# Performance work log

Measured on AMD Instinct MI355X. Metric: run time of the kernel, lower is better.

## Reference

```python
import jax, jax.numpy as jnp
import numpy as np

N_HEAD = 16
HEAD_DIM = 128
HIDDEN = 2048
ROPE_BASE = 10000.0
RMS_EPS = 1e-5


def _rms_norm(t, w, eps=RMS_EPS):
    # RMSNorm over last dim with learned scale
    var = jnp.mean(jnp.square(t), axis=-1, keepdims=True)
    return t * jax.lax.rsqrt(var + eps) * w


def _rope_cos_sin(T, dim, base=ROPE_BASE, dtype=jnp.float32):
    inv_freq = 1.0 / (base ** (jnp.arange(0, dim, 2, dtype=jnp.float32) / dim))
    pos = jnp.arange(T, dtype=jnp.float32)
    freqs = pos[:, None] * inv_freq[None, :]  # [T, dim/2]
    return jnp.cos(freqs).astype(dtype), jnp.sin(freqs).astype(dtype)


def _apply_rotary(t, cos, sin):
    # t: [B, T, H, D]; rotate-half (GPT-NeoX style)
    d2 = t.shape[-1] // 2
    t1, t2 = t[..., :d2], t[..., d2:]
    c = cos[None, :, None, :]
    s = sin[None, :, None, :]
    return jnp.concatenate([t1 * c - t2 * s, t1 * s + t2 * c], axis=-1)


def setup_inputs() -> dict:
    key = jax.random.key(0)
    ks = jax.random.split(key, 7)
    B, T = 2, 2048
    w_std = 1.0 / np.sqrt(HIDDEN)
    proj_std = 0.5 / np.sqrt(HIDDEN) / np.sqrt(24)  # hidden_init_std_factor / sqrt(H) / sqrt(L)
    return {
        "x": jax.random.normal(ks[0], (B, T, HIDDEN), jnp.float32),
        "Wq": jax.random.normal(ks[1], (HIDDEN, N_HEAD * HEAD_DIM), jnp.float32) * w_std,
        "Wk": jax.random.normal(ks[2], (HIDDEN, N_HEAD * HEAD_DIM), jnp.float32) * w_std,
        "Wv": jax.random.normal(ks[3], (HIDDEN, N_HEAD * HEAD_DIM), jnp.float32) * w_std,
        "Wg": jax.random.normal(ks[4], (HIDDEN, N_HEAD * HEAD_DIM), jnp.float32) * w_std,
        "Wo": jax.random.normal(ks[5], (N_HEAD * HEAD_DIM, HIDDEN), jnp.float32) * proj_std,
        "q_rms_w": jnp.ones((HEAD_DIM,), jnp.float32),
        "k_rms_w": jnp.ones((HEAD_DIM,), jnp.float32),
        "o_norm_w": jnp.ones((HEAD_DIM,), jnp.float32),
    }


def reference(x, Wq, Wk, Wv, Wg, Wo, q_rms_w, k_rms_w, o_norm_w):
    B, T, _ = x.shape
    H, D = N_HEAD, HEAD_DIM

    q = (x @ Wq).reshape(B, T, H, D)
    k = (x @ Wk).reshape(B, T, H, D)
    v = (x @ Wv).reshape(B, T, H, D)

    # RoPE (no past, offset = 0)
    cos, sin = _rope_cos_sin(T, D, dtype=x.dtype)
    q = _apply_rotary(q, cos, sin)
    k = _apply_rotary(k, cos, sin)

    # QK RMSNorm (per-head-dim affine)
    q = _rms_norm(q, q_rms_w)
    k = _rms_norm(k, k_rms_w)

    # causal SDPA
    scale = 1.0 / np.sqrt(D)
    scores = jnp.einsum("bqhd,bkhd->bhqk", q, k) * scale
    causal = jnp.tril(jnp.ones((T, T), dtype=bool))
    scores = jnp.where(causal[None, None, :, :], scores, jnp.finfo(scores.dtype).min)
    probs = jax.nn.softmax(scores, axis=-1)
    y = jnp.einsum("bhqk,bkhd->bqhd", probs, v)  # [B, T, H, D]

    # output norm + silu gate
    y = _rms_norm(y, o_norm_w)
    gate = (x @ Wg).reshape(B, T, H, D)
    y = y * jax.nn.silu(gate)

    y = y.reshape(B, T, H * D)
    return y @ Wo
```

## Files before the change

### kernel.cpp

```cpp
#include <hip/hip_runtime.h>
#include <hip/hip_bf16.h>
#include <stdint.h>

typedef __bf16 bf16x8 __attribute__((ext_vector_type(8)));
typedef float f32x4 __attribute__((ext_vector_type(4)));
typedef __hip_bfloat16 bf16;

__device__ __forceinline__ void gload16(const void* g, void* l) {
    __builtin_amdgcn_global_load_lds(
        (const __attribute__((address_space(1))) uint32_t*)g,
        (__attribute__((address_space(3))) uint32_t*)l,
        16, 0, 0);
}

__global__ void k_cvt_bf16(const float* __restrict__ in, bf16* __restrict__ out, int n4) {
    int i = blockIdx.x * blockDim.x + threadIdx.x;
    if (i >= n4) return;
    float4 v = reinterpret_cast<const float4*>(in)[i];
    union { bf16 h[4]; uint2 u; } pk;
    pk.h[0] = __float2bfloat16(v.x);
    pk.h[1] = __float2bfloat16(v.y);
    pk.h[2] = __float2bfloat16(v.z);
    pk.h[3] = __float2bfloat16(v.w);
    reinterpret_cast<uint2*>(out)[i] = pk.u;
}

__global__ void k_rope_tbl(float* __restrict__ tbl) {
    int i = blockIdx.x * blockDim.x + threadIdx.x;
    int t = i >> 6, j = i & 63;
    float inv = powf(10000.0f, -(float)j * (1.0f / 64.0f));
    float f = (float)t * inv;
    tbl[t * 128 + j] = cosf(f);
    tbl[t * 128 + 64 + j] = sinf(f);
}

__global__ void k_wtrans(const float* __restrict__ w0, const float* __restrict__ w1,
                         const float* __restrict__ w2, const float* __restrict__ w3,
                         const float* __restrict__ w4, bf16* __restrict__ out) {
    __shared__ float tile[32][33];
    const float* srcs[5] = {w0, w1, w2, w3, w4};
    const float* src = srcs[blockIdx.z];
    bf16* dst = out + (size_t)blockIdx.z * 2048 * 2048;
    int k0 = blockIdx.x * 32, n0 = blockIdx.y * 32;
    int tx = threadIdx.x, ty = threadIdx.y;
#pragma unroll
    for (int i = 0; i < 4; i++)
        tile[ty + 8 * i][tx] = src[(size_t)(k0 + ty + 8 * i) * 2048 + n0 + tx];
    __syncthreads();
#pragma unroll
    for (int i = 0; i < 4; i++)
        dst[(size_t)(n0 + ty + 8 * i) * 2048 + k0 + tx] = __float2bfloat16(tile[tx][ty + 8 * i]);
}

__global__ __launch_bounds__(256) void k_gemm(
    const bf16* __restrict__ A, const bf16* __restrict__ Bt, float* __restrict__ C,
    int M, int N, int K) {
    __shared__ __align__(16) bf16 As[128 * 64];
    __shared__ __align__(16) bf16 Bs[128 * 64];
    int lane = threadIdx.x & 63, wave = threadIdx.x >> 6;
    int g = lane >> 4, cc = lane & 15;
    int wr = wave >> 1, wc = wave & 1;
    size_t m0 = (size_t)blockIdx.x * 128, n0 = (size_t)blockIdx.y * 128;
    const bf16* Ab = A + m0 * K;
    const bf16* Bb = Bt + (size_t)blockIdx.z * N * K + n0 * K;
    float* Cb = C + (size_t)blockIdx.z * M * N + m0 * N + n0;

    f32x4 acc[4][4];
#pragma unroll
    for (int i = 0; i < 4; i++)
#pragma unroll
        for (int j = 0; j < 4; j++) acc[i][j] = {0.f, 0.f, 0.f, 0.f};

    int scol = (lane & 7) * 8;
    for (int k0 = 0; k0 < K; k0 += 64) {
#pragma unroll
        for (int i = 0; i < 4; i++) {
            int ch = wave * 4 + i;
            int row = ch * 8 + (lane >> 3);
            gload16(&Ab[(size_t)row * K + k0 + scol], &As[ch * 512]);
            gload16(&Bb[(size_t)row * K + k0 + scol], &Bs[ch * 512]);
        }
        __syncthreads();
#pragma unroll
        for (int kk = 0; kk < 2; kk++) {
            bf16x8 af[4], bfr[4];
#pragma unroll
            for (int m = 0; m < 4; m++)
                af[m] = *reinterpret_cast<const bf16x8*>(&As[(wr * 64 + m * 16 + cc) * 64 + kk * 32 + g * 8]);
#pragma unroll
            for (int n = 0; n < 4; n++)
                bfr[n] = *reinterpret_cast<const bf16x8*>(&Bs[(wc * 64 + n * 16 + cc) * 64 + kk * 32 + g * 8]);
#pragma unroll
            for (int m = 0; m < 4; m++)
#pragma unroll
                for (int n = 0; n < 4; n++)
                    acc[m][n] = __builtin_amdgcn_mfma_f32_16x16x32_bf16(af[m], bfr[n], acc[m][n], 0, 0, 0);
        }
        __syncthreads();
    }
#pragma unroll
    for (int m = 0; m < 4; m++)
#pragma unroll
        for (int n = 0; n < 4; n++)
#pragma unroll
            for (int r = 0; r < 4; r++) {
                size_t row = wr * 64 + m * 16 + g * 4 + r;
                Cb[row * N + (wc * 64 + n * 16 + cc)] = acc[m][n][r];
            }
}

__global__ __launch_bounds__(512, 2) void k_gemm256(
    const bf16* __restrict__ A, const bf16* __restrict__ Bt, bf16* __restrict__ C,
    int M, int N, int K) {
    __shared__ __align__(16) bf16 lds[2][8][64 * 64];
    const int tid = threadIdx.x;
    const int lane = tid & 63, wave = tid >> 6;
    const int g = lane >> 4, c = lane & 15, cx = c & 7;
    const int wr = wave >> 2, wc = wave & 3;
    const int id = blockIdx.x;
    const int swz = (id & 7) * 64 + (id >> 3);
    const int xt = swz & 15, yt = (swz >> 4) & 7, zt = swz >> 7;
    const size_t m0 = (size_t)xt * 256, n0 = (size_t)yt * 256;
    const bf16* Ab = A + m0 * K;
    const bf16* Bb = Bt + (size_t)zt * (size_t)N * K + n0 * K;
    bf16* Cb = C + (size_t)zt * (size_t)M * N + m0 * N + n0;
    const int nt = K >> 6;

    const int srow = tid >> 3;
    const int scol = ((tid & 7) ^ (srow & 7)) * 8;

    auto stage = [&](int u, int q) {
        if (u >= nt) return;
        const bf16* src = (q < 4) ? &Ab[(size_t)(q * 64 + srow) * K]
                                  : &Bb[(size_t)((q - 4) * 64 + srow) * K];
        gload16(&src[((size_t)u << 6) + scol], &lds[u & 1][q][wave * 512]);
    };

    f32x4 acc[8][4];
#pragma unroll
    for (int i = 0; i < 8; i++)
#pragma unroll
        for (int j = 0; j < 4; j++) acc[i][j] = {0.f, 0.f, 0.f, 0.f};

#pragma unroll
    for (int q = 0; q < 8; q++) stage(0, q);
    stage(1, 0); stage(1, 2); stage(1, 4); stage(1, 5); stage(1, 6); stage(1, 7);
    asm volatile("s_waitcnt vmcnt(6)" ::: "memory");
    __builtin_amdgcn_s_barrier();

    bf16x8 afr[4][2], bfr[2][2][2];

#define READ_A(mh)                                                                   \
    do {                                                                             \
        const bf16* aq = &lds[t & 1][wr * 2 + (mh)][0];                              \
        _Pragma("unroll") for (int m_ = 0; m_ < 4; m_++)                             \
            _Pragma("unroll") for (int kh = 0; kh < 2; kh++)                         \
                afr[m_][kh] = *reinterpret_cast<const bf16x8*>(                      \
                    aq + (m_ * 16 + c) * 64 + ((kh * 4 + g) ^ cx) * 8);              \
    } while (0)
#define READ_B(nh)                                                                   \
    do {                                                                             \
        const bf16* bq = &lds[t & 1][4 + wc][0];                                     \
        _Pragma("unroll") for (int n_ = 0; n_ < 2; n_++)                             \
            _Pragma("unroll") for (int kh = 0; kh < 2; kh++)                         \
                bfr[nh][n_][kh] = *reinterpret_cast<const bf16x8*>(                  \
                    bq + (((nh)*2 + n_) * 16 + c) * 64 + ((kh * 4 + g) ^ cx) * 8);   \
    } while (0)
#define QUAD(mh, nh)                                                                 \
    do {                                                                             \
        __builtin_amdgcn_s_setprio(1);                                               \
        _Pragma("unroll") for (int kh = 0; kh < 2; kh++)                             \
            _Pragma("unroll") for (int m_ = 0; m_ < 4; m_++)                         \
                _Pragma("unroll") for (int n_ = 0; n_ < 2; n_++)                     \
                    acc[(mh)*4 + m_][(nh)*2 + n_] =                                  \
                        __builtin_amdgcn_mfma_f32_16x16x32_bf16(                     \
                            afr[m_][kh], bfr[nh][n_][kh],                            \
                            acc[(mh)*4 + m_][(nh)*2 + n_], 0, 0, 0);                 \
        __builtin_amdgcn_s_setprio(0);                                               \
    } while (0)

    for (int t = 0; t < nt; ++t) {
        READ_A(0);
        READ_B(0);
        stage(t + 1, 1); stage(t + 1, 3);
        __builtin_amdgcn_s_barrier();
        asm volatile("s_waitcnt lgkmcnt(0)" ::: "memory");
        __builtin_amdgcn_sched_barrier(0);
        QUAD(0, 0);
        __builtin_amdgcn_s_barrier();
        READ_B(1);
        stage(t + 2, 0); stage(t + 2, 2);
        __builtin_amdgcn_s_barrier();
        asm volatile("s_waitcnt lgkmcnt(0)" ::: "memory");
        __builtin_amdgcn_sched_barrier(0);
        QUAD(0, 1);
        __builtin_amdgcn_s_barrier();
        READ_A(1);
        stage(t + 2, 4); stage(t + 2, 5);
        __builtin_amdgcn_s_barrier();
        asm volatile("s_waitcnt lgkmcnt(0)" ::: "memory");
        __builtin_amdgcn_sched_barrier(0);
        QUAD(1, 0);
        __builtin_amdgcn_s_barrier();
        stage(t + 2, 6); stage(t + 2, 7);
        if (t < nt - 2) asm volatile("s_waitcnt vmcnt(6)" ::: "memory");
        else            asm volatile("s_waitcnt vmcnt(0)" ::: "memory");
        __builtin_amdgcn_s_barrier();
        __builtin_amdgcn_sched_barrier(0);
        QUAD(1, 1);
        __builtin_amdgcn_s_barrier();
    }
#undef READ_A
#undef READ_B
#undef QUAD
#pragma unroll
    for (int m_ = 0; m_ < 8; m_++)
#pragma unroll
        for (int n_ = 0; n_ < 4; n_++)
#pragma unroll
            for (int r_ = 0; r_ < 4; r_++) {
                size_t row = wr * 128 + m_ * 16 + g * 4 + r_;
                Cb[row * N + wc * 64 + n_ * 16 + c] = __float2bfloat16(acc[m_][n_][r_]);
            }
}

__global__ void k_rope_rms(const bf16* __restrict__ src, const float* __restrict__ rmsw,
                           const float* __restrict__ tbl, bf16* __restrict__ dst,
                           float outscale) {
    const int T = 2048;
    int wv = blockIdx.x * 4 + (threadIdx.x >> 6);
    int lane = threadIdx.x & 63;
    int h = wv & 15, bt = wv >> 4;
    int t = bt & (T - 1), b_ = bt >> 11;
    const bf16* p = src + (size_t)bt * 2048 + h * 128;
    float a = __bfloat162float(p[lane]), b = __bfloat162float(p[lane + 64]);
    float cs = tbl[t * 128 + lane], sn = tbl[t * 128 + 64 + lane];
    float r1 = a * cs - b * sn, r2 = a * sn + b * cs;
    float ss = r1 * r1 + r2 * r2;
#pragma unroll
    for (int d = 1; d < 64; d <<= 1) ss += __shfl_xor(ss, d, 64);
    float rs = rsqrtf(ss * (1.0f / 128.0f) + 1e-5f);
    size_t o = ((size_t)(b_ * 16 + h) * T + t) * 128;
    dst[o + lane] = __float2bfloat16(r1 * rs * rmsw[lane] * outscale);
    dst[o + lane + 64] = __float2bfloat16(r2 * rs * rmsw[lane + 64] * outscale);
}

__global__ void k_vtrans(const bf16* __restrict__ V, bf16* __restrict__ Vt) {
    const int T = 2048;
    __shared__ float tile[32][33];
    int bh = blockIdx.z, b_ = bh >> 4, h = bh & 15;
    int t0 = blockIdx.x * 32, d0 = blockIdx.y * 32;
    int tx = threadIdx.x, ty = threadIdx.y;
#pragma unroll
    for (int i = 0; i < 4; i++)
        tile[ty + 8 * i][tx] =
            __bfloat162float(V[((size_t)(b_ * T + t0 + ty + 8 * i)) * 2048 + h * 128 + d0 + tx]);
    __syncthreads();
#pragma unroll
    for (int i = 0; i < 4; i++)
        Vt[((size_t)bh * 128 + d0 + ty + 8 * i) * T + t0 + tx] = __float2bfloat16(tile[tx][ty + 8 * i]);
}

__global__ __launch_bounds__(256) void k_attn(
    const bf16* __restrict__ Q, const bf16* __restrict__ K,
    const bf16* __restrict__ Vt, float* __restrict__ Y) {
    const int T = 2048;
    __shared__ __align__(16) bf16 KsB[2][64 * 128];
    __shared__ __align__(16) bf16 VsB[2][128 * 64];
    __shared__ __align__(16) bf16 Ps[64 * 72];
    int lane = threadIdx.x & 63, wave = threadIdx.x >> 6;
    int g = lane >> 4, c = lane & 15;
    int wg = blockIdx.x;
    int bh = wg & 31;
    int qt = 31 - (wg >> 5);
    int q0 = qt * 64;
    const bf16* Qb = Q + (size_t)bh * T * 128;
    const bf16* Kb = K + (size_t)bh * T * 128;
    const bf16* Vb = Vt + (size_t)bh * 128 * T;

    int qrow = q0 + wave * 16 + c;
    bf16x8 qf[4];
#pragma unroll
    for (int kk = 0; kk < 4; kk++)
        qf[kk] = *reinterpret_cast<const bf16x8*>(&Qb[(size_t)qrow * 128 + kk * 32 + g * 8]);

    int kli = lane >> 4;
    int vli = lane >> 3;
    int vlu = (lane & 7) ^ (vli & 7);

    auto stage = [&](int kv0, int b) {
#pragma unroll
        for (int i = 0; i < 4; i++) {
            int ch = wave * 4 + i;
            int krow = ch * 4 + kli;
            int klu = (lane & 15) ^ (krow & 7);
            gload16(&Kb[(size_t)(kv0 + krow) * 128 + klu * 8], &KsB[b][ch * 512]);
            int vrow = ch * 8 + vli;
            gload16(&Vb[(size_t)vrow * T + kv0 + vlu * 8], &VsB[b][ch * 512]);
        }
    };

    f32x4 acc[8];
#pragma unroll
    for (int i = 0; i < 8; i++) acc[i] = {0.f, 0.f, 0.f, 0.f};
    float m = -INFINITY, l = 0.f;

    int ntiles = qt + 1;
    stage(0, 0);
    __syncthreads();
    int cur = 0;
    for (int it = 0; it < ntiles; ++it) {
        int kv0 = it * 64;
        if (it + 1 < ntiles) stage(kv0 + 64, cur ^ 1);
        const bf16* Ks = KsB[cur];
        const bf16* Vs = VsB[cur];

        f32x4 s[4];
#pragma unroll
        for (int nf = 0; nf < 4; nf++) s[nf] = {0.f, 0.f, 0.f, 0.f};
#pragma unroll
        for (int nf = 0; nf < 4; nf++)
#pragma unroll
            for (int kk = 0; kk < 4; kk++) {
                int pu = (kk * 4 + g) ^ (c & 7);
                bf16x8 kf = *reinterpret_cast<const bf16x8*>(&Ks[(nf * 16 + c) * 128 + pu * 8]);
                s[nf] = __builtin_amdgcn_mfma_f32_16x16x32_bf16(kf, qf[kk], s[nf], 0, 0, 0);
            }
        if (it == ntiles - 1) {
#pragma unroll
            for (int nf = 0; nf < 4; nf++)
#pragma unroll
                for (int r = 0; r < 4; r++)
                    if (kv0 + nf * 16 + g * 4 + r > qrow) s[nf][r] = -1e30f;
        }
        float mx = -INFINITY;
#pragma unroll
        for (int nf = 0; nf < 4; nf++)
#pragma unroll
            for (int r = 0; r < 4; r++) mx = fmaxf(mx, s[nf][r]);
        mx = fmaxf(mx, __shfl_xor(mx, 16, 64));
        mx = fmaxf(mx, __shfl_xor(mx, 32, 64));
        float mnew = fmaxf(m, mx);
        float alpha = __expf(m - mnew);
        m = mnew;
        float rsum = 0.f;
#pragma unroll
        for (int nf = 0; nf < 4; nf++)
#pragma unroll
            for (int r = 0; r < 4; r++) {
                float p = __expf(s[nf][r] - mnew);
                s[nf][r] = p;
                rsum += p;
            }
        rsum += __shfl_xor(rsum, 16, 64);
        rsum += __shfl_xor(rsum, 32, 64);
        l = l * alpha + rsum;
        float al[4];
#pragma unroll
        for (int r = 0; r < 4; r++) al[r] = __shfl(alpha, g * 4 + r, 64);
#pragma unroll
        for (int nf = 0; nf < 8; nf++)
#pragma unroll
            for (int r = 0; r < 4; r++) acc[nf][r] *= al[r];
#pragma unroll
        for (int nf = 0; nf < 4; nf++) {
            union { bf16 h[4]; uint2 u; } pk;
#pragma unroll
            for (int r = 0; r < 4; r++) pk.h[r] = __float2bfloat16(s[nf][r]);
            *reinterpret_cast<uint2*>(&Ps[(wave * 16 + c) * 72 + nf * 16 + g * 4]) = pk.u;
        }
#pragma unroll
        for (int kk2 = 0; kk2 < 2; kk2++) {
            bf16x8 pf = *reinterpret_cast<const bf16x8*>(&Ps[(wave * 16 + c) * 72 + kk2 * 32 + g * 8]);
#pragma unroll
            for (int nf = 0; nf < 8; nf++) {
                int pu = (kk2 * 4 + g) ^ (c & 7);
                bf16x8 vf = *reinterpret_cast<const bf16x8*>(&Vs[(nf * 16 + c) * 64 + pu * 8]);
                acc[nf] = __builtin_amdgcn_mfma_f32_16x16x32_bf16(pf, vf, acc[nf], 0, 0, 0);
            }
        }
        __syncthreads();
        cur ^= 1;
    }
    float inv = 1.0f / l;
    float iv[4];
#pragma unroll
    for (int r = 0; r < 4; r++) iv[r] = __shfl(inv, g * 4 + r, 64);
#pragma unroll
    for (int r = 0; r < 4; r++) {
        size_t row = q0 + wave * 16 + g * 4 + r;
#pragma unroll
        for (int nf = 0; nf < 8; nf++)
            Y[(size_t)bh * T * 128 + row * 128 + nf * 16 + c] = acc[nf][r] * iv[r];
    }
}

__global__ void k_finalize(const float* __restrict__ Y, const bf16* __restrict__ gate,
                           const float* __restrict__ ow, bf16* __restrict__ out) {
    const int T = 2048;
    int wv = blockIdx.x * 4 + (threadIdx.x >> 6);
    int lane = threadIdx.x & 63;
    int t = wv & (T - 1), bh = wv >> 11;
    int b_ = bh >> 4, h = bh & 15;
    const float* y = Y + (size_t)wv * 128;
    float y1 = y[lane], y2 = y[lane + 64];
    float ss = y1 * y1 + y2 * y2;
#pragma unroll
    for (int d = 1; d < 64; d <<= 1) ss += __shfl_xor(ss, d, 64);
    float rs = rsqrtf(ss * (1.0f / 128.0f) + 1e-5f);
    size_t gi = ((size_t)(b_ * T + t)) * 2048 + h * 128;
    float g1 = __bfloat162float(gate[gi + lane]), g2 = __bfloat162float(gate[gi + lane + 64]);
    g1 = g1 / (1.f + __expf(-g1));
    g2 = g2 / (1.f + __expf(-g2));
    out[gi + lane] = __float2bfloat16(y1 * rs * ow[lane] * g1);
    out[gi + lane + 64] = __float2bfloat16(y2 * rs * ow[lane + 64] * g2);
}

extern "C" void kernel_launch(void* const* d_in, const int* in_sizes, int n_in,
                              void* d_out, int out_size, void* d_ws, size_t ws_size,
                              hipStream_t stream) {
    const float* x  = (const float*)d_in[0];
    const float* Wq = (const float*)d_in[1];
    const float* Wk = (const float*)d_in[2];
    const float* Wv = (const float*)d_in[3];
    const float* Wg = (const float*)d_in[4];
    const float* Wo = (const float*)d_in[5];
    const float* qw = (const float*)d_in[6];
    const float* kw = (const float*)d_in[7];
    const float* ow = (const float*)d_in[8];

    const size_t M = 4096, HID = 2048;
    char* w = (char*)d_ws;
    bf16*  xb    = (bf16*)(w);
    bf16*  Wt    = (bf16*)(w + 16777216);
    bf16*  qkvg  = (bf16*)(w + 58720256);
    bf16*  q_att = (bf16*)(w + 125829120);
    bf16*  k_att = (bf16*)(w + 142606336);
    bf16*  vt    = (bf16*)(w + 159383552);
    float* tbl   = (float*)(w + 176160768);
    float* y_att = (float*)(w + 177209344);
    bf16*  yg    = (bf16*)(w + 210763776);

    k_cvt_bf16<<<8192, 256, 0, stream>>>(x, xb, (int)(M * HID / 4));
    k_rope_tbl<<<512, 256, 0, stream>>>(tbl);
    k_wtrans<<<dim3(64, 64, 5), dim3(32, 8), 0, stream>>>(Wq, Wk, Wv, Wg, Wo, Wt);
    k_gemm256<<<512, 512, 0, stream>>>(xb, Wt, qkvg, (int)M, 2048, 2048);
    k_rope_rms<<<16384, 256, 0, stream>>>(qkvg, qw, tbl, q_att, 0.08838834764831845f);
    k_rope_rms<<<16384, 256, 0, stream>>>(qkvg + M * HID, kw, tbl, k_att, 1.0f);
    k_vtrans<<<dim3(64, 4, 32), dim3(32, 8), 0, stream>>>(qkvg + 2 * M * HID, vt);
    k_attn<<<1024, 256, 0, stream>>>(q_att, k_att, vt, y_att);
    k_finalize<<<16384, 256, 0, stream>>>(y_att, qkvg + 3 * M * HID, ow, yg);
    k_gemm<<<dim3(32, 16, 1), 256, 0, stream>>>(yg, Wt + (size_t)4 * 2048 * 2048, (float*)d_out,
                                                (int)M, 2048, 2048);
}
```

Before: 327.9 us.

## Prefetch LDS fragments across quadrants and reuse 256-tile GEMM for output projection

The 256x256 GEMM main loop now double-buffers A fragments in registers (afr0/afr1) and issues the next tile's LDS reads before the last MFMA quadrant. It waits on partial lgkmcnt counts instead of draining to zero, so LDS reads overlap with MFMA work. The kernel is templated on output type with generic tile swizzling, and the simple 128x128 output-projection GEMM is replaced by this pipelined kernel writing fp32. This raises register pressure, and the final GEMM runs only 128 blocks, which may underfill the GPU.

Result: slower. 337.3 us (+2.9%).

```diff
diff --git a/kernel.cpp b/kernel.cpp
--- a/kernel.cpp
+++ b/kernel.cpp
@@ -52,78 +52,24 @@
         dst[(size_t)(n0 + ty + 8 * i) * 2048 + k0 + tx] = __float2bfloat16(tile[tx][ty + 8 * i]);
 }
 
-__global__ __launch_bounds__(256) void k_gemm(
-    const bf16* __restrict__ A, const bf16* __restrict__ Bt, float* __restrict__ C,
-    int M, int N, int K) {
-    __shared__ __align__(16) bf16 As[128 * 64];
-    __shared__ __align__(16) bf16 Bs[128 * 64];
-    int lane = threadIdx.x & 63, wave = threadIdx.x >> 6;
-    int g = lane >> 4, cc = lane & 15;
-    int wr = wave >> 1, wc = wave & 1;
-    size_t m0 = (size_t)blockIdx.x * 128, n0 = (size_t)blockIdx.y * 128;
-    const bf16* Ab = A + m0 * K;
-    const bf16* Bb = Bt + (size_t)blockIdx.z * N * K + n0 * K;
-    float* Cb = C + (size_t)blockIdx.z * M * N + m0 * N + n0;
-
-    f32x4 acc[4][4];
-#pragma unroll
-    for (int i = 0; i < 4; i++)
-#pragma unroll
-        for (int j = 0; j < 4; j++) acc[i][j] = {0.f, 0.f, 0.f, 0.f};
-
-    int scol = (lane & 7) * 8;
-    for (int k0 = 0; k0 < K; k0 += 64) {
-#pragma unroll
-        for (int i = 0; i < 4; i++) {
-            int ch = wave * 4 + i;
-            int row = ch * 8 + (lane >> 3);
-            gload16(&Ab[(size_t)row * K + k0 + scol], &As[ch * 512]);
-            gload16(&Bb[(size_t)row * K + k0 + scol], &Bs[ch * 512]);
-        }
-        __syncthreads();
-#pragma unroll
-        for (int kk = 0; kk < 2; kk++) {
-            bf16x8 af[4], bfr[4];
-#pragma unroll
-            for (int m = 0; m < 4; m++)
-                af[m] = *reinterpret_cast<const bf16x8*>(&As[(wr * 64 + m * 16 + cc) * 64 + kk * 32 + g * 8]);
-#pragma unroll
-            for (int n = 0; n < 4; n++)
-                bfr[n] = *reinterpret_cast<const bf16x8*>(&Bs[(wc * 64 + n * 16 + cc) * 64 + kk * 32 + g * 8]);
-#pragma unroll
-            for (int m = 0; m < 4; m++)
-#pragma unroll
-                for (int n = 0; n < 4; n++)
-                    acc[m][n] = __builtin_amdgcn_mfma_f32_16x16x32_bf16(af[m], bfr[n], acc[m][n], 0, 0, 0);
-        }
-        __syncthreads();
-    }
-#pragma unroll
-    for (int m = 0; m < 4; m++)
-#pragma unroll
-        for (int n = 0; n < 4; n++)
-#pragma unroll
-            for (int r = 0; r < 4; r++) {
-                size_t row = wr * 64 + m * 16 + g * 4 + r;
-                Cb[row * N + (wc * 64 + n * 16 + cc)] = acc[m][n][r];
-            }
-}
-
+template <typename OutT>
 __global__ __launch_bounds__(512, 2) void k_gemm256(
-    const bf16* __restrict__ A, const bf16* __restrict__ Bt, bf16* __restrict__ C,
+    const bf16* __restrict__ A, const bf16* __restrict__ Bt, OutT* __restrict__ C,
     int M, int N, int K) {
     __shared__ __align__(16) bf16 lds[2][8][64 * 64];
     const int tid = threadIdx.x;
     const int lane = tid & 63, wave = tid >> 6;
     const int g = lane >> 4, c = lane & 15, cx = c & 7;
     const int wr = wave >> 2, wc = wave & 3;
+    const int Mt = M >> 8, Nt = N >> 8;
+    const int cpx = (int)gridDim.x >> 3;
     const int id = blockIdx.x;
-    const int swz = (id & 7) * 64 + (id >> 3);
-    const int xt = swz & 15, yt = (swz >> 4) & 7, zt = swz >> 7;
+    const int swz = (id & 7) * cpx + (id >> 3);
+    const int xt = swz % Mt, yt = (swz / Mt) % Nt, zt = swz / (Mt * Nt);
     const size_t m0 = (size_t)xt * 256, n0 = (size_t)yt * 256;
     const bf16* Ab = A + m0 * K;
     const bf16* Bb = Bt + (size_t)zt * (size_t)N * K + n0 * K;
-    bf16* Cb = C + (size_t)zt * (size_t)M * N + m0 * N + n0;
+    OutT* Cb = C + (size_t)zt * (size_t)M * N + m0 * N + n0;
     const int nt = K >> 6;
 
     const int srow = tid >> 3;
@@ -142,31 +88,25 @@
 #pragma unroll
         for (int j = 0; j < 4; j++) acc[i][j] = {0.f, 0.f, 0.f, 0.f};
 
-#pragma unroll
-    for (int q = 0; q < 8; q++) stage(0, q);
-    stage(1, 0); stage(1, 2); stage(1, 4); stage(1, 5); stage(1, 6); stage(1, 7);
-    asm volatile("s_waitcnt vmcnt(6)" ::: "memory");
-    __builtin_amdgcn_s_barrier();
-
-    bf16x8 afr[4][2], bfr[2][2][2];
-
-#define READ_A(mh)                                                                   \
+    bf16x8 afr0[4][2], afr1[4][2], bfr[2][2][2];
+
+#define READ_A(dst, bufi, mh)                                                        \
     do {                                                                             \
-        const bf16* aq = &lds[t & 1][wr * 2 + (mh)][0];                              \
+        const bf16* aq = &lds[bufi][wr * 2 + (mh)][0];                               \
         _Pragma("unroll") for (int m_ = 0; m_ < 4; m_++)                             \
             _Pragma("unroll") for (int kh = 0; kh < 2; kh++)                         \
-                afr[m_][kh] = *reinterpret_cast<const bf16x8*>(                      \
+                dst[m_][kh] = *reinterpret_cast<const bf16x8*>(                      \
                     aq + (m_ * 16 + c) * 64 + ((kh * 4 + g) ^ cx) * 8);              \
     } while (0)
-#define READ_B(nh)                                                                   \
+#define READ_B(nh, bufi)                                                             \
     do {                                                                             \
-        const bf16* bq = &lds[t & 1][4 + wc][0];                                     \
+        const bf16* bq = &lds[bufi][4 + wc][0];                                      \
         _Pragma("unroll") for (int n_ = 0; n_ < 2; n_++)                             \
             _Pragma("unroll") for (int kh = 0; kh < 2; kh++)                         \
                 bfr[nh][n_][kh] = *reinterpret_cast<const bf16x8*>(                  \
                     bq + (((nh)*2 + n_) * 16 + c) * 64 + ((kh * 4 + g) ^ cx) * 8);   \
     } while (0)
-#define QUAD(mh, nh)                                                                 \
+#define QUADX(Aset, mh, nh)                                                          \
     do {                                                                             \
         __builtin_amdgcn_s_setprio(1);                                               \
         _Pragma("unroll") for (int kh = 0; kh < 2; kh++)                             \
@@ -174,45 +114,56 @@
                 _Pragma("unroll") for (int n_ = 0; n_ < 2; n_++)                     \
                     acc[(mh)*4 + m_][(nh)*2 + n_] =                                  \
                         __builtin_amdgcn_mfma_f32_16x16x32_bf16(                     \
-                            afr[m_][kh], bfr[nh][n_][kh],                            \
+                            Aset[m_][kh], bfr[nh][n_][kh],                           \
                             acc[(mh)*4 + m_][(nh)*2 + n_], 0, 0, 0);                 \
         __builtin_amdgcn_s_setprio(0);                                               \
     } while (0)
 
+#pragma unroll
+    for (int q = 0; q < 8; q++) stage(0, q);
+    stage(1, 0); stage(1, 2); stage(1, 4); stage(1, 5); stage(1, 6); stage(1, 7);
+    asm volatile("s_waitcnt vmcnt(6)" ::: "memory");
+    __builtin_amdgcn_s_barrier();
+    READ_A(afr0, 0, 0);
+    READ_B(0, 0);
+
     for (int t = 0; t < nt; ++t) {
-        READ_A(0);
-        READ_B(0);
+        const int bi = t & 1;
+        READ_B(1, bi);
         stage(t + 1, 1); stage(t + 1, 3);
+        __builtin_amdgcn_s_barrier();
+        asm volatile("s_waitcnt lgkmcnt(4)" ::: "memory");
+        __builtin_amdgcn_sched_barrier(0);
+        QUADX(afr0, 0, 0);
+        __builtin_amdgcn_s_barrier();
+        READ_A(afr1, bi, 1);
+        stage(t + 2, 0); stage(t + 2, 2);
+        __builtin_amdgcn_s_barrier();
+        asm volatile("s_waitcnt lgkmcnt(8)" ::: "memory");
+        __builtin_amdgcn_sched_barrier(0);
+        QUADX(afr0, 0, 1);
+        __builtin_amdgcn_s_barrier();
+        stage(t + 2, 4); stage(t + 2, 5);
         __builtin_amdgcn_s_barrier();
         asm volatile("s_waitcnt lgkmcnt(0)" ::: "memory");
         __builtin_amdgcn_sched_barrier(0);
-        QUAD(0, 0);
-        __builtin_amdgcn_s_barrier();
-        READ_B(1);
-        stage(t + 2, 0); stage(t + 2, 2);
-        __builtin_amdgcn_s_barrier();
-        asm volatile("s_waitcnt lgkmcnt(0)" ::: "memory");
-        __builtin_amdgcn_sched_barrier(0);
-        QUAD(0, 1);
-        __builtin_amdgcn_s_barrier();
-        READ_A(1);
-        stage(t + 2, 4); stage(t + 2, 5);
-        __builtin_amdgcn_s_barrier();
-        asm volatile("s_waitcnt lgkmcnt(0)" ::: "memory");
-        __builtin_amdgcn_sched_barrier(0);
-        QUAD(1, 0);
+        QUADX(afr1, 1, 0);
         __builtin_amdgcn_s_barrier();
         stage(t + 2, 6); stage(t + 2, 7);
         if (t < nt - 2) asm volatile("s_waitcnt vmcnt(6)" ::: "memory");
         else            asm volatile("s_waitcnt vmcnt(0)" ::: "memory");
         __builtin_amdgcn_s_barrier();
+        if (t + 1 < nt) {
+            READ_A(afr0, (t + 1) & 1, 0);
+            READ_B(0, (t + 1) & 1);
+        }
         __builtin_amdgcn_sched_barrier(0);
-        QUAD(1, 1);
+        QUADX(afr1, 1, 1);
         __builtin_amdgcn_s_barrier();
     }
 #undef READ_A
 #undef READ_B
-#undef QUAD
+#undef QUADX
 #pragma unroll
     for (int m_ = 0; m_ < 8; m_++)
 #pragma unroll
@@ -220,7 +171,10 @@
 #pragma unroll
             for (int r_ = 0; r_ < 4; r_++) {
                 size_t row = wr * 128 + m_ * 16 + g * 4 + r_;
-                Cb[row * N + wc * 64 + n_ * 16 + c] = __float2bfloat16(acc[m_][n_][r_]);
+                if constexpr (sizeof(OutT) == 2)
+                    Cb[row * N + wc * 64 + n_ * 16 + c] = __float2bfloat16(acc[m_][n_][r_]);
+                else
+                    Cb[row * N + wc * 64 + n_ * 16 + c] = acc[m_][n_][r_];
             }
 }
 
@@ -444,12 +398,12 @@
     k_cvt_bf16<<<8192, 256, 0, stream>>>(x, xb, (int)(M * HID / 4));
     k_rope_tbl<<<512, 256, 0, stream>>>(tbl);
     k_wtrans<<<dim3(64, 64, 5), dim3(32, 8), 0, stream>>>(Wq, Wk, Wv, Wg, Wo, Wt);
-    k_gemm256<<<512, 512, 0, stream>>>(xb, Wt, qkvg, (int)M, 2048, 2048);
+    k_gemm256<bf16><<<512, 512, 0, stream>>>(xb, Wt, qkvg, (int)M, 2048, 2048);
     k_rope_rms<<<16384, 256, 0, stream>>>(qkvg, qw, tbl, q_att, 0.08838834764831845f);
     k_rope_rms<<<16384, 256, 0, stream>>>(qkvg + M * HID, kw, tbl, k_att, 1.0f);
     k_vtrans<<<dim3(64, 4, 32), dim3(32, 8), 0, stream>>>(qkvg + 2 * M * HID, vt);
     k_attn<<<1024, 256, 0, stream>>>(q_att, k_att, vt, y_att);
     k_finalize<<<16384, 256, 0, stream>>>(y_att, qkvg + 3 * M * HID, ow, yg);
-    k_gemm<<<dim3(32, 16, 1), 256, 0, stream>>>(yg, Wt + (size_t)4 * 2048 * 2048, (float*)d_out,
-                                                (int)M, 2048, 2048);
-}
+    k_gemm256<float><<<128, 512, 0, stream>>>(yg, Wt + (size_t)4 * 2048 * 2048, (float*)d_out,
+                                              (int)M, 2048, 2048);
+}
```

## Use 32-wide KV tiles with per-wave causal skip and bf16 attention output

Applied to the files above, without the earlier changes.

The attention loop now processes KV in 32-key tiles with a smaller shared-memory footprint and a new V swizzle, and each wave skips tiles that lie entirely above its own causal diagonal. Masking applies only to tiles that straddle the diagonal. The attention output is written as bf16 instead of fp32, which halves the intermediate traffic read by the finalize kernel. In exchange there are twice as many loop iterations with a barrier each, and the output is stored at lower precision before the RMS norm.

After: 341.3 us. 4.1% more time.

```diff
diff --git a/kernel.cpp b/kernel.cpp
--- a/kernel.cpp
+++ b/kernel.cpp
@@ -263,11 +263,11 @@
 
 __global__ __launch_bounds__(256) void k_attn(
     const bf16* __restrict__ Q, const bf16* __restrict__ K,
-    const bf16* __restrict__ Vt, float* __restrict__ Y) {
+    const bf16* __restrict__ Vt, bf16* __restrict__ Y) {
     const int T = 2048;
-    __shared__ __align__(16) bf16 KsB[2][64 * 128];
-    __shared__ __align__(16) bf16 VsB[2][128 * 64];
-    __shared__ __align__(16) bf16 Ps[64 * 72];
+    __shared__ __align__(16) bf16 KsB[2][32 * 128];
+    __shared__ __align__(16) bf16 VsB[2][128 * 32];
+    __shared__ __align__(16) bf16 Ps[64 * 40];
     int lane = threadIdx.x & 63, wave = threadIdx.x >> 6;
     int g = lane >> 4, c = lane & 15;
     int wg = blockIdx.x;
@@ -285,17 +285,17 @@
         qf[kk] = *reinterpret_cast<const bf16x8*>(&Qb[(size_t)qrow * 128 + kk * 32 + g * 8]);
 
     int kli = lane >> 4;
-    int vli = lane >> 3;
-    int vlu = (lane & 7) ^ (vli & 7);
+    int vri = lane >> 2;
 
     auto stage = [&](int kv0, int b) {
 #pragma unroll
-        for (int i = 0; i < 4; i++) {
-            int ch = wave * 4 + i;
+        for (int i = 0; i < 2; i++) {
+            int ch = wave * 2 + i;
             int krow = ch * 4 + kli;
             int klu = (lane & 15) ^ (krow & 7);
             gload16(&Kb[(size_t)(kv0 + krow) * 128 + klu * 8], &KsB[b][ch * 512]);
-            int vrow = ch * 8 + vli;
+            int vrow = ch * 16 + vri;
+            int vlu = (lane & 3) ^ ((vrow >> 1) & 3);
             gload16(&Vb[(size_t)vrow * T + kv0 + vlu * 8], &VsB[b][ch * 512]);
         }
     };
@@ -305,77 +305,72 @@
     for (int i = 0; i < 8; i++) acc[i] = {0.f, 0.f, 0.f, 0.f};
     float m = -INFINITY, l = 0.f;
 
-    int ntiles = qt + 1;
+    int ntiles = 2 * qt + 2;
     stage(0, 0);
     __syncthreads();
     int cur = 0;
     for (int it = 0; it < ntiles; ++it) {
-        int kv0 = it * 64;
-        if (it + 1 < ntiles) stage(kv0 + 64, cur ^ 1);
-        const bf16* Ks = KsB[cur];
-        const bf16* Vs = VsB[cur];
-
-        f32x4 s[4];
-#pragma unroll
-        for (int nf = 0; nf < 4; nf++) s[nf] = {0.f, 0.f, 0.f, 0.f};
-#pragma unroll
-        for (int nf = 0; nf < 4; nf++)
-#pragma unroll
-            for (int kk = 0; kk < 4; kk++) {
-                int pu = (kk * 4 + g) ^ (c & 7);
-                bf16x8 kf = *reinterpret_cast<const bf16x8*>(&Ks[(nf * 16 + c) * 128 + pu * 8]);
-                s[nf] = __builtin_amdgcn_mfma_f32_16x16x32_bf16(kf, qf[kk], s[nf], 0, 0, 0);
+        int kv0 = it * 32;
+        if (it + 1 < ntiles) stage(kv0 + 32, cur ^ 1);
+        if (kv0 <= q0 + wave * 16 + 15) {
+            const bf16* Ks = KsB[cur];
+            const bf16* Vs = VsB[cur];
+            f32x4 s[2];
+#pragma unroll
+            for (int nf = 0; nf < 2; nf++) s[nf] = {0.f, 0.f, 0.f, 0.f};
+#pragma unroll
+            for (int nf = 0; nf < 2; nf++)
+#pragma unroll
+                for (int kk = 0; kk < 4; kk++) {
+                    int pu = (kk * 4 + g) ^ (c & 7);
+                    bf16x8 kf = *reinterpret_cast<const bf16x8*>(&Ks[(nf * 16 + c) * 128 + pu * 8]);
+                    s[nf] = __builtin_amdgcn_mfma_f32_16x16x32_bf16(kf, qf[kk], s[nf], 0, 0, 0);
+                }
+            if (kv0 + 31 > q0 + wave * 16) {
+#pragma unroll
+                for (int nf = 0; nf < 2; nf++)
+#pragma unroll
+                    for (int r = 0; r < 4; r++)
+                        if (kv0 + nf * 16 + g * 4 + r > qrow) s[nf][r] = -1e30f;
             }
-        if (it == ntiles - 1) {
-#pragma unroll
-            for (int nf = 0; nf < 4; nf++)
-#pragma unroll
-                for (int r = 0; r < 4; r++)
-                    if (kv0 + nf * 16 + g * 4 + r > qrow) s[nf][r] = -1e30f;
-        }
-        float mx = -INFINITY;
-#pragma unroll
-        for (int nf = 0; nf < 4; nf++)
-#pragma unroll
-            for (int r = 0; r < 4; r++) mx = fmaxf(mx, s[nf][r]);
-        mx = fmaxf(mx, __shfl_xor(mx, 16, 64));
-        mx = fmaxf(mx, __shfl_xor(mx, 32, 64));
-        float mnew = fmaxf(m, mx);
-        float alpha = __expf(m - mnew);
-        m = mnew;
-        float rsum = 0.f;
-#pragma unroll
-        for (int nf = 0; nf < 4; nf++)
-#pragma unroll
-            for (int r = 0; r < 4; r++) {
-                float p = __expf(s[nf][r] - mnew);
-                s[nf][r] = p;
-                rsum += p;
+            float mx = fmaxf(fmaxf(fmaxf(s[0][0], s[0][1]), fmaxf(s[0][2], s[0][3])),
+                             fmaxf(fmaxf(s[1][0], s[1][1]), fmaxf(s[1][2], s[1][3])));
+            mx = fmaxf(mx, __shfl_xor(mx, 16, 64));
+            mx = fmaxf(mx, __shfl_xor(mx, 32, 64));
+            float mnew = fmaxf(m, mx);
+            float alpha = __expf(m - mnew);
+            m = mnew;
+            float rsum = 0.f;
+#pragma unroll
+            for (int nf = 0; nf < 2; nf++)
+#pragma unroll
+                for (int r = 0; r < 4; r++) {
+                    float p = __expf(s[nf][r] - mnew);
+                    s[nf][r] = p;
+                    rsum += p;
+                }
+            rsum += __shfl_xor(rsum, 16, 64);
+            rsum += __shfl_xor(rsum, 32, 64);
+            l = l * alpha + rsum;
+            float al[4];
+#pragma unroll
+            for (int r = 0; r < 4; r++) al[r] = __shfl(alpha, g * 4 + r, 64);
+#pragma unroll
+            for (int nf = 0; nf < 8; nf++)
+#pragma unroll
+                for (int r = 0; r < 4; r++) acc[nf][r] *= al[r];
+#pragma unroll
+            for (int nf = 0; nf < 2; nf++) {
+                union { bf16 h[4]; uint2 u; } pk;
+#pragma unroll
+                for (int r = 0; r < 4; r++) pk.h[r] = __float2bfloat16(s[nf][r]);
+                *reinterpret_cast<uint2*>(&Ps[(wave * 16 + c) * 40 + nf * 16 + g * 4]) = pk.u;
             }
-        rsum += __shfl_xor(rsum, 16, 64);
-        rsum += __shfl_xor(rsum, 32, 64);
-        l = l * alpha + rsum;
-        float al[4];
-#pragma unroll
-        for (int r = 0; r < 4; r++) al[r] = __shfl(alpha, g * 4 + r, 64);
-#pragma unroll
-        for (int nf = 0; nf < 8; nf++)
-#pragma unroll
-            for (int r = 0; r < 4; r++) acc[nf][r] *= al[r];
-#pragma unroll
-        for (int nf = 0; nf < 4; nf++) {
-            union { bf16 h[4]; uint2 u; } pk;
-#pragma unroll
-            for (int r = 0; r < 4; r++) pk.h[r] = __float2bfloat16(s[nf][r]);
-            *reinterpret_cast<uint2*>(&Ps[(wave * 16 + c) * 72 + nf * 16 + g * 4]) = pk.u;
-        }
-#pragma unroll
-        for (int kk2 = 0; kk2 < 2; kk2++) {
-            bf16x8 pf = *reinterpret_cast<const bf16x8*>(&Ps[(wave * 16 + c) * 72 + kk2 * 32 + g * 8]);
+            bf16x8 pf = *reinterpret_cast<const bf16x8*>(&Ps[(wave * 16 + c) * 40 + g * 8]);
 #pragma unroll
             for (int nf = 0; nf < 8; nf++) {
-                int pu = (kk2 * 4 + g) ^ (c & 7);
-                bf16x8 vf = *reinterpret_cast<const bf16x8*>(&Vs[(nf * 16 + c) * 64 + pu * 8]);
+                int pu = g ^ ((c >> 1) & 3);
+                bf16x8 vf = *reinterpret_cast<const bf16x8*>(&Vs[(nf * 16 + c) * 32 + pu * 8]);
                 acc[nf] = __builtin_amdgcn_mfma_f32_16x16x32_bf16(pf, vf, acc[nf], 0, 0, 0);
             }
         }
@@ -391,19 +386,20 @@
         size_t row = q0 + wave * 16 + g * 4 + r;
 #pragma unroll
         for (int nf = 0; nf < 8; nf++)
-            Y[(size_t)bh * T * 128 + row * 128 + nf * 16 + c] = acc[nf][r] * iv[r];
+            Y[(size_t)bh * T * 128 + row * 128 + nf * 16 + c] =
+                __float2bfloat16(acc[nf][r] * iv[r]);
     }
 }
 
-__global__ void k_finalize(const float* __restrict__ Y, const bf16* __restrict__ gate,
+__global__ void k_finalize(const bf16* __restrict__ Y, const bf16* __restrict__ gate,
                            const float* __restrict__ ow, bf16* __restrict__ out) {
     const int T = 2048;
     int wv = blockIdx.x * 4 + (threadIdx.x >> 6);
     int lane = threadIdx.x & 63;
     int t = wv & (T - 1), bh = wv >> 11;
     int b_ = bh >> 4, h = bh & 15;
-    const float* y = Y + (size_t)wv * 128;
-    float y1 = y[lane], y2 = y[lane + 64];
+    const bf16* y = Y + (size_t)wv * 128;
+    float y1 = __bfloat162float(y[lane]), y2 = __bfloat162float(y[lane + 64]);
     float ss = y1 * y1 + y2 * y2;
 #pragma unroll
     for (int d = 1; d < 64; d <<= 1) ss += __shfl_xor(ss, d, 64);
@@ -438,7 +434,7 @@
     bf16*  k_att = (bf16*)(w + 142606336);
     bf16*  vt    = (bf16*)(w + 159383552);
     float* tbl   = (float*)(w + 176160768);
-    float* y_att = (float*)(w + 177209344);
+    bf16*  y_att = (bf16*)(w + 177209344);
     bf16*  yg    = (bf16*)(w + 210763776);
 
     k_cvt_bf16<<<8192, 256, 0, stream>>>(x, xb, (int)(M * HID / 4));
```
